# Performance work log

Hardware: AMD Instinct MI355X
Metric: run time of the kernel (lower is better)

Reference implementation:

```python
import jax, jax.numpy as jnp
import numpy as np
import math

N_HEAD = 16  # from init_kwargs

def setup_inputs() -> dict:
    key = jax.random.key(0)
    ks = jax.random.split(key, 11)
    B, T, D = 2, 2048, 1024
    s = 0.02
    return {
        "q": jax.random.normal(ks[0], (B, T, D), jnp.float32),
        "k": jax.random.normal(ks[1], (B, T, D), jnp.float32),
        "v": jax.random.normal(ks[2], (B, T, D), jnp.float32),
        "Wq": jax.random.normal(ks[3], (D, D), jnp.float32) * s,
        "bq": jax.random.normal(ks[4], (D,), jnp.float32) * s,
        "Wk": jax.random.normal(ks[5], (D, D), jnp.float32) * s,
        "bk": jax.random.normal(ks[6], (D,), jnp.float32) * s,
        "Wv": jax.random.normal(ks[7], (D, D), jnp.float32) * s,
        "bv": jax.random.normal(ks[8], (D,), jnp.float32) * s,
        "Wc": jax.random.normal(ks[9], (D, D), jnp.float32) * s,
        "bc": jax.random.normal(ks[10], (D,), jnp.float32) * s,
    }

def reference(q, k, v, Wq, bq, Wk, bk, Wv, bv, Wc, bc):
    B, T, D = q.shape
    H = N_HEAD
    nd = D // H

    def proj(x, W, b):
        # torch Linear: x @ W.T + b; then split heads -> [b, h, t, nd]
        y = x @ W.T + b
        return y.reshape(B, T, H, nd).transpose(0, 2, 1, 3)

    qh = proj(q, Wq, bq)
    kh = proj(k, Wk, bk)
    vh = proj(v, Wv, bv)

    # scores: [b, h, t_q, t_k]
    z = jnp.einsum('bhqd,bhkd->bhqk', qh, kh) / math.sqrt(nd)
    mask = jnp.tril(jnp.ones((T, T), dtype=bool))  # causal
    z = jnp.where(mask, z, -jnp.inf)
    # NOTE: original uses nn.Softmax(dim=-2) -> softmax over the QUERY axis
    attn = jax.nn.softmax(z, axis=-2)
    out = jnp.einsum('bhqk,bhkd->bhqd', attn, vh)  # [b, h, t, nd]
    out = out.transpose(0, 2, 1, 3).reshape(B, T, D)
    return out @ Wc.T + bc
```

## Files before the change

### kernel.cpp

```cpp
#include <hip/hip_runtime.h>


#define Dd 1024
#define Tt 2048
#define Bb 2
#define Hh 16
#define NDh 64
#define Mm (Bb * Tt)
#define LOG2E 1.44269504f

using u16 = unsigned short;
using u32 = unsigned int;
typedef __attribute__((ext_vector_type(8))) short bf16x8;
typedef __attribute__((ext_vector_type(4))) short bf16x4;
typedef __attribute__((ext_vector_type(4))) float f32x4;

__device__ __forceinline__ u16 f2bf(float f) {
  return (u16)((__float_as_uint(f) + 0x8000u) >> 16);
}
__device__ __forceinline__ float exp2_hw(float x) {
  float r; asm("v_exp_f32 %0, %1" : "=v"(r) : "v"(x)); return r;
}
__device__ __forceinline__ u32 cvtpk(float lo, float hi) {
  u32 r; asm("v_cvt_pk_bf16_f32 %0, %1, %2" : "=v"(r) : "v"(lo), "v"(hi));
  return r;
}
__device__ __forceinline__ void ldsdma16(const u16* g, u16* l) {
  __builtin_amdgcn_global_load_lds(
      (const __attribute__((address_space(1))) u32*)g,
      (__attribute__((address_space(3))) u32*)l, 16, 0, 0);
}
#define MFMA(a, b, c) __builtin_amdgcn_mfma_f32_16x16x32_bf16((a), (b), (c), 0, 0, 0)
__device__ __forceinline__ f32x4 mfma16(bf16x4 a, bf16x4 b, f32x4 c) {
#if __has_builtin(__builtin_amdgcn_mfma_f32_16x16x16bf16_1k)
  return __builtin_amdgcn_mfma_f32_16x16x16bf16_1k(a, b, c, 0, 0, 0);
#else
  f32x4 d;
  asm("v_mfma_f32_16x16x16_bf16 %0, %1, %2, %3"
      : "=v"(d) : "v"(a), "v"(b), "0"(c));
  return d;
#endif
}
__device__ __forceinline__ bf16x8 ldfrag(const u16* lds, int row, int kgrp) {
  return *(const bf16x8*)(lds + row * 64 + (((kgrp) ^ (row & 7)) * 8));
}
__device__ __forceinline__ bf16x4 ldv4(const u16* lds, int row, int e0) {
  return *(const bf16x4*)(lds + row * 64 + (((e0 >> 3) ^ (row & 7)) * 8) + (e0 & 7));
}

__global__ __launch_bounds__(256) void cvt_all(
    const float* __restrict__ w0, const float* __restrict__ w1,
    const float* __restrict__ w2, const float* __restrict__ w3,
    const float* __restrict__ xq, const float* __restrict__ xk,
    const float* __restrict__ xv,
    u16* __restrict__ Wb, u16* __restrict__ Qb, u16* __restrict__ Kb,
    u16* __restrict__ Vb, float* __restrict__ outz, float* __restrict__ lsumz)
{
  const int vid = blockIdx.x * 256 + threadIdx.x;
  const int seg = vid >> 18;
  const size_t off = (size_t)(vid & 0x3FFFF) * 4;
  const float* s;
  u16* d;
  if (seg < 4) {
    s = seg == 0 ? w0 : seg == 1 ? w1 : seg == 2 ? w2 : w3;
    d = Wb + (size_t)seg * Dd * Dd;
  } else {
    const int xi = (seg - 4) >> 2;
    const size_t xo = (size_t)((seg - 4) & 3) << 20;
    s = (xi == 0 ? xq : xi == 1 ? xk : xv) + xo;
    d = (xi == 0 ? Qb : xi == 1 ? Kb : Vb) + xo;
  }
  float4 f = *(const float4*)(s + off);
  ushort4 o;
  o.x = f2bf(f.x); o.y = f2bf(f.y); o.z = f2bf(f.z); o.w = f2bf(f.w);
  *(ushort4*)(d + off) = o;
  if (vid < Mm * Dd / 4)
    *(float4*)(outz + (size_t)vid * 4) = make_float4(0.f, 0.f, 0.f, 0.f);
  if (vid < Bb * Hh * Tt / 4)
    *(float4*)(lsumz + (size_t)vid * 4) = make_float4(0.f, 0.f, 0.f, 0.f);
}

__device__ __forceinline__ void gemm_body(
    const u16* __restrict__ X, const u16* __restrict__ WB,
    const float* __restrict__ bias, void* Yv, float oscale, int omode,
    int kc, int knum, u16* As, u16* Bs)
{
  const int t = threadIdx.x, lane = t & 63, w = t >> 6;
  const int col = lane & 15, quad = lane >> 4;
  const int m0 = blockIdx.x * 64, n0 = blockIdx.y * 128;
  const int wm = (w >> 1) * 32, wn = (w & 1) * 64;
  const int drr = lane >> 3, dsw = ((lane & 7) ^ drr) * 8;
  const int kbeg = (Dd / knum) * kc, kend = kbeg + Dd / knum;

  f32x4 acc[2][4] = {};

  for (int k0 = kbeg; k0 < kend; k0 += 64) {
    __syncthreads();
#pragma unroll
    for (int i = 0; i < 2; i++) {
      const int rr = w * 16 + i * 8;
      ldsdma16(X + (size_t)(m0 + rr + drr) * Dd + k0 + dsw, As + rr * 64);
    }
#pragma unroll
    for (int i = 0; i < 4; i++) {
      const int rr = w * 32 + i * 8;
      ldsdma16(WB + (size_t)(n0 + rr + drr) * Dd + k0 + dsw, Bs + rr * 64);
    }
    __syncthreads();
#pragma unroll
    for (int s = 0; s < 2; s++) {
      bf16x8 a[2], b[4];
#pragma unroll
      for (int i = 0; i < 2; i++)
        a[i] = ldfrag(As, wm + i * 16 + col, s * 4 + quad);
#pragma unroll
      for (int j = 0; j < 4; j++)
        b[j] = ldfrag(Bs, wn + j * 16 + col, s * 4 + quad);
#pragma unroll
      for (int i = 0; i < 2; i++)
#pragma unroll
        for (int j = 0; j < 4; j++)
          acc[i][j] = MFMA(a[i], b[j], acc[i][j]);
    }
  }

#pragma unroll
  for (int jt = 0; jt < 4; jt++) {
    const int n = n0 + wn + jt * 16 + col;
    const float bn = (omode == 2 && kc != 0) ? 0.f : bias[n];
    if (omode == 1) {
#pragma unroll
      for (int i = 0; i < 2; i++) {
        const int mg = m0 + wm + i * 16 + quad * 4;
        const int bb = mg >> 11, tl = mg & 2047;
        ushort4 o;
        o.x = f2bf(acc[i][jt][0] + bn);
        o.y = f2bf(acc[i][jt][1] + bn);
        o.z = f2bf(acc[i][jt][2] + bn);
        o.w = f2bf(acc[i][jt][3] + bn);
        *(ushort4*)((u16*)Yv + (size_t)bb * Dd * Tt + (size_t)n * Tt + tl) = o;
      }
    } else if (omode == 0) {
      u16* Y = (u16*)Yv;
#pragma unroll
      for (int i = 0; i < 2; i++)
#pragma unroll
        for (int r = 0; r < 4; r++) {
          const int m = m0 + wm + i * 16 + quad * 4 + r;
          Y[(size_t)m * Dd + n] = f2bf((acc[i][jt][r] + bn) * oscale);
        }
    } else {
      float* Y = (float*)Yv;
#pragma unroll
      for (int i = 0; i < 2; i++)
#pragma unroll
        for (int r = 0; r < 4; r++) {
          const int m = m0 + wm + i * 16 + quad * 4 + r;
          atomicAdd(&Y[(size_t)m * Dd + n], acc[i][jt][r] + bn);
        }
    }
  }
}

__global__ __launch_bounds__(256) void proj_qkv(
    const u16* __restrict__ Qb, const u16* __restrict__ Kb,
    const u16* __restrict__ Vb, const u16* __restrict__ Wb,
    const float* __restrict__ bq, const float* __restrict__ bk,
    const float* __restrict__ bv,
    u16* __restrict__ Qp, u16* __restrict__ Kp, u16* __restrict__ VtG)
{
  __shared__ u16 As[64 * 64];
  __shared__ u16 Bs[128 * 64];
  const int z = blockIdx.z;
  const u16* X = z == 0 ? Qb : z == 1 ? Kb : Vb;
  const u16* W = Wb + (size_t)z * Dd * Dd;
  const float* bias = z == 0 ? bq : z == 1 ? bk : bv;
  void* Y = z == 0 ? (void*)Qp : z == 1 ? (void*)Kp : (void*)VtG;
  gemm_body(X, W, bias, Y, z == 0 ? 0.125f * LOG2E : 1.0f, z == 2 ? 1 : 0,
            0, 1, As, Bs);
}

__global__ __launch_bounds__(256) void gemm_final(
    const u16* __restrict__ Ctx, const u16* __restrict__ Wcb,
    const float* __restrict__ bc, float* __restrict__ out)
{
  __shared__ u16 As[64 * 64];
  __shared__ u16 Bs[128 * 64];
  gemm_body(Ctx, Wcb, bc, out, 1.0f, 2, blockIdx.z, 2, As, Bs);
}

__global__ __launch_bounds__(256) void attn_stats(
    const u16* __restrict__ Qp, const u16* __restrict__ Kp,
    float* __restrict__ lsum)
{
  __shared__ u16 Ks[128 * 64];
  __shared__ u16 Qs[64 * 64];
  const int t = threadIdx.x, lane = t & 63, w = t >> 6;
  const int col = lane & 15, quad = lane >> 4;
  const int bh = blockIdx.x, b = bh >> 4, h = bh & 15;
  const int j = blockIdx.y, tk0 = j * 128, c = blockIdx.z;
  const u16* Kbase = Kp + (size_t)b * Tt * Dd + h * NDh;
  const u16* Qbase = Qp + (size_t)b * Tt * Dd + h * NDh;
  const int drr = lane >> 3, dsw = ((lane & 7) ^ drr) * 8;

#pragma unroll
  for (int i = 0; i < 4; i++) {
    const int rr = w * 32 + i * 8;
    ldsdma16(Kbase + (size_t)(tk0 + rr + drr) * Dd + dsw, Ks + rr * 64);
  }
  __syncthreads();
  bf16x8 ka[2][2];
#pragma unroll
  for (int s2 = 0; s2 < 2; s2++) {
    const int row = w * 32 + s2 * 16 + col;
    ka[s2][0] = ldfrag(Ks, row, quad);
    ka[s2][1] = ldfrag(Ks, row, 4 + quad);
  }

  float l[2][4] = {};

  for (int d = 2 * j + c, i0 = 0; d < Tt / 64; d += 4, i0++) {
    const bool masked = (c < 2) && (i0 == 0);
    const int tq0 = d * 64;
    __syncthreads();
#pragma unroll
    for (int i = 0; i < 2; i++) {
      const int rr = w * 16 + i * 8;
      ldsdma16(Qbase + (size_t)(tq0 + rr + drr) * Dd + dsw, Qs + rr * 64);
    }
    __syncthreads();
#pragma unroll
    for (int jt = 0; jt < 4; jt++) {
      bf16x8 qb0 = ldfrag(Qs, jt * 16 + col, quad);
      bf16x8 qb1 = ldfrag(Qs, jt * 16 + col, 4 + quad);
      const int tq = tq0 + jt * 16 + col;
#pragma unroll
      for (int s2 = 0; s2 < 2; s2++) {
        f32x4 z = {};
        z = MFMA(ka[s2][0], qb0, z);
        z = MFMA(ka[s2][1], qb1, z);
#pragma unroll
        for (int r = 0; r < 4; r++) {
          float e = exp2_hw(z[r]);
          if (masked) {
            const int tk = tk0 + w * 32 + s2 * 16 + quad * 4 + r;
            e = (tq >= tk) ? e : 0.f;
          }
          l[s2][r] += e;
        }
      }
    }
  }

#pragma unroll
  for (int s2 = 0; s2 < 2; s2++)
#pragma unroll
    for (int r = 0; r < 4; r++) {
      float s = l[s2][r];
#pragma unroll
      for (int m = 1; m < 16; m <<= 1) s += __shfl_xor(s, m);
      if (col == 0)
        atomicAdd(&lsum[(size_t)bh * Tt + tk0 + w * 32 + s2 * 16 + quad * 4 + r], s);
    }
}

__global__ __launch_bounds__(256) void attn_out(
    const u16* __restrict__ Qp, const u16* __restrict__ Kp,
    const u16* __restrict__ VtG, const float* __restrict__ lsum,
    u16* __restrict__ Ctx)
{
  __shared__ u16 Ks[2][64 * 64];
  __shared__ u16 Vts[2][64 * 64];
  __shared__ float srl[2][64];
  const int t = threadIdx.x, lane = t & 63, w = t >> 6;
  const int col = lane & 15, quad = lane >> 4;
  const int bh = blockIdx.x, b = bh >> 4, h = bh & 15;
  const int tq0 = (gridDim.y - 1 - blockIdx.y) * 64;
  const u16* Qbase = Qp + (size_t)b * Tt * Dd + h * NDh;
  const u16* Kbase = Kp + (size_t)b * Tt * Dd + h * NDh;
  const u16* Vbase = VtG + (size_t)b * Dd * Tt + (size_t)h * NDh * Tt;
  const int drr = lane >> 3, dsw = ((lane & 7) ^ drr) * 8;

#pragma unroll
  for (int i = 0; i < 2; i++) {
    const int rr = w * 16 + i * 8;
    ldsdma16(Qbase + (size_t)(tq0 + rr + drr) * Dd + dsw, Ks[0] + rr * 64);
  }
  __syncthreads();
  bf16x8 qa0 = ldfrag(Ks[0], w * 16 + col, quad);
  bf16x8 qa1 = ldfrag(Ks[0], w * 16 + col, 4 + quad);

  f32x4 o[4] = {};

  auto compute = [&](const u16* Kc, const u16* Vc, const float* rlc,
                     bool masked) {
#pragma unroll
    for (int jt = 0; jt < 4; jt++) {
      bf16x8 kb0 = ldfrag(Kc, jt * 16 + col, quad);
      bf16x8 kb1 = ldfrag(Kc, jt * 16 + col, 4 + quad);
      f32x4 z = {};
      z = MFMA(kb0, qa0, z);
      z = MFMA(kb1, qa1, z);
      const f32x4 rl = *(const f32x4*)(rlc + jt * 16 + quad * 4);
      float p0 = exp2_hw(z[0]) * rl[0];
      float p1 = exp2_hw(z[1]) * rl[1];
      float p2 = exp2_hw(z[2]) * rl[2];
      float p3 = exp2_hw(z[3]) * rl[3];
      if (masked) {
        const int tkb = jt * 16 + quad * 4, tq = w * 16 + col;
        p0 = (tkb + 0 <= tq) ? p0 : 0.f;
        p1 = (tkb + 1 <= tq) ? p1 : 0.f;
        p2 = (tkb + 2 <= tq) ? p2 : 0.f;
        p3 = (tkb + 3 <= tq) ? p3 : 0.f;
      }
      u32 pk01 = cvtpk(p0, p1), pk23 = cvtpk(p2, p3);
      u32 pkv[2] = {pk01, pk23};
      const bf16x4 pb2 = *(const bf16x4*)pkv;
#pragma unroll
      for (int dn = 0; dn < 4; dn++) {
        const bf16x4 va = ldv4(Vc, dn * 16 + col, jt * 16 + quad * 4);
        o[dn] = mfma16(va, pb2, o[dn]);
      }
    }
  };

  for (int tk0 = 0; tk0 <= tq0; tk0 += 128) {
    const bool two = (tk0 + 64 <= tq0);
    __syncthreads();
#pragma unroll
    for (int i = 0; i < 2; i++) {
      const int rr = w * 16 + i * 8;
      ldsdma16(Kbase + (size_t)(tk0 + rr + drr) * Dd + dsw, Ks[0] + rr * 64);
      ldsdma16(Vbase + (size_t)(rr + drr) * Tt + tk0 + dsw, Vts[0] + rr * 64);
    }
    if (two) {
#pragma unroll
      for (int i = 0; i < 2; i++) {
        const int rr = w * 16 + i * 8;
        ldsdma16(Kbase + (size_t)(tk0 + 64 + rr + drr) * Dd + dsw,
                 Ks[1] + rr * 64);
        ldsdma16(Vbase + (size_t)(rr + drr) * Tt + tk0 + 64 + dsw,
                 Vts[1] + rr * 64);
      }
    }
    if (t < 64) {
      srl[0][t] = 1.0f / lsum[(size_t)bh * Tt + tk0 + t];
      if (two) srl[1][t] = 1.0f / lsum[(size_t)bh * Tt + tk0 + 64 + t];
    }
    __syncthreads();
    compute(Ks[0], Vts[0], srl[0], tk0 == tq0);
    if (two) compute(Ks[1], Vts[1], srl[1], tk0 + 64 == tq0);
  }

#pragma unroll
  for (int dn = 0; dn < 4; dn++) {
    ushort4 ov;
    ov.x = f2bf(o[dn][0]); ov.y = f2bf(o[dn][1]);
    ov.z = f2bf(o[dn][2]); ov.w = f2bf(o[dn][3]);
    *(ushort4*)(Ctx + (size_t)(b * Tt + tq0 + w * 16 + col) * Dd +
                h * NDh + dn * 16 + quad * 4) = ov;
  }
}

extern "C" void kernel_launch(void* const* d_in, const int* in_sizes, int n_in,
                              void* d_out, int out_size, void* d_ws, size_t ws_size,
                              hipStream_t stream)
{
  const float* q  = (const float*)d_in[0];
  const float* k  = (const float*)d_in[1];
  const float* v  = (const float*)d_in[2];
  const float* Wq = (const float*)d_in[3];
  const float* bq = (const float*)d_in[4];
  const float* Wk = (const float*)d_in[5];
  const float* bk = (const float*)d_in[6];
  const float* Wv = (const float*)d_in[7];
  const float* bv = (const float*)d_in[8];
  const float* Wc = (const float*)d_in[9];
  const float* bc = (const float*)d_in[10];

  u16* Wb   = (u16*)d_ws;
  u16* Qp   = Wb + (size_t)4 * Dd * Dd;
  u16* Kp   = Qp + (size_t)Mm * Dd;
  u16* VtG  = Kp + (size_t)Mm * Dd;
  u16* Ctx  = VtG + (size_t)Mm * Dd;
  float* lsum = (float*)(Ctx + (size_t)Mm * Dd);
  u16* Qb   = (u16*)(lsum + (size_t)Bb * Hh * Tt);
  u16* Kb   = Qb + (size_t)Mm * Dd;
  u16* Vb   = Ctx;

  cvt_all<<<16384, 256, 0, stream>>>(Wq, Wk, Wv, Wc, q, k, v,
                                     Wb, Qb, Kb, Vb, (float*)d_out, lsum);
  proj_qkv<<<dim3(Mm / 64, Dd / 128, 3), 256, 0, stream>>>(
      Qb, Kb, Vb, Wb, bq, bk, bv, Qp, Kp, VtG);
  attn_stats<<<dim3(Bb * Hh, Tt / 128, 4), 256, 0, stream>>>(Qp, Kp, lsum);
  attn_out<<<dim3(Bb * Hh, Tt / 64), 256, 0, stream>>>(Qp, Kp, VtG, lsum, Ctx);
  gemm_final<<<dim3(Mm / 64, Dd / 128, 2), 256, 0, stream>>>(
      Ctx, Wb + (size_t)3 * Dd * Dd, bc, (float*)d_out);
}
```

Before: 257.9 us.

## Pair short and long causal query tiles per block in attn_out

Each attn_out block now handles two 64-row query tiles, p and 31-p, so every block does about the same causal work. The K/V tiles loaded into shared memory are reused for both query tiles, and the grid shrinks from 32 to 16 blocks per head. This removes tail imbalance and halves K/V reloads, but it doubles accumulator registers and leaves 512 blocks, which may hurt occupancy and latency hiding.

Result: no change. 257.8 us (-0.0%).

```diff
diff --git a/kernel.cpp b/kernel.cpp
--- a/kernel.cpp
+++ b/kernel.cpp
@@ -275,7 +275,8 @@
   const int t = threadIdx.x, lane = t & 63, w = t >> 6;
   const int col = lane & 15, quad = lane >> 4;
   const int bh = blockIdx.x, b = bh >> 4, h = bh & 15;
-  const int tq0 = (gridDim.y - 1 - blockIdx.y) * 64;
+  const int p = blockIdx.y;
+  const int tqA = p * 64, tqB = (31 - p) * 64;
   const u16* Qbase = Qp + (size_t)b * Tt * Dd + h * NDh;
   const u16* Kbase = Kp + (size_t)b * Tt * Dd + h * NDh;
   const u16* Vbase = VtG + (size_t)b * Dd * Tt + (size_t)h * NDh * Tt;
@@ -284,48 +285,76 @@
 #pragma unroll
   for (int i = 0; i < 2; i++) {
     const int rr = w * 16 + i * 8;
-    ldsdma16(Qbase + (size_t)(tq0 + rr + drr) * Dd + dsw, Ks[0] + rr * 64);
+    ldsdma16(Qbase + (size_t)(tqA + rr + drr) * Dd + dsw, Ks[0] + rr * 64);
+    ldsdma16(Qbase + (size_t)(tqB + rr + drr) * Dd + dsw, Ks[1] + rr * 64);
   }
   __syncthreads();
-  bf16x8 qa0 = ldfrag(Ks[0], w * 16 + col, quad);
-  bf16x8 qa1 = ldfrag(Ks[0], w * 16 + col, 4 + quad);
-
-  f32x4 o[4] = {};
-
-  auto compute = [&](const u16* Kc, const u16* Vc, const float* rlc,
-                     bool masked) {
+  bf16x8 qaA0 = ldfrag(Ks[0], w * 16 + col, quad);
+  bf16x8 qaA1 = ldfrag(Ks[0], w * 16 + col, 4 + quad);
+  bf16x8 qaB0 = ldfrag(Ks[1], w * 16 + col, quad);
+  bf16x8 qaB1 = ldfrag(Ks[1], w * 16 + col, 4 + quad);
+
+  f32x4 oA[4] = {}, oB[4] = {};
+
+  auto computePair = [&](const u16* Kc, const u16* Vc, const float* rlc,
+                         bool actA, bool mA, bool mB) {
 #pragma unroll
     for (int jt = 0; jt < 4; jt++) {
       bf16x8 kb0 = ldfrag(Kc, jt * 16 + col, quad);
       bf16x8 kb1 = ldfrag(Kc, jt * 16 + col, 4 + quad);
-      f32x4 z = {};
-      z = MFMA(kb0, qa0, z);
-      z = MFMA(kb1, qa1, z);
       const f32x4 rl = *(const f32x4*)(rlc + jt * 16 + quad * 4);
-      float p0 = exp2_hw(z[0]) * rl[0];
-      float p1 = exp2_hw(z[1]) * rl[1];
-      float p2 = exp2_hw(z[2]) * rl[2];
-      float p3 = exp2_hw(z[3]) * rl[3];
-      if (masked) {
-        const int tkb = jt * 16 + quad * 4, tq = w * 16 + col;
-        p0 = (tkb + 0 <= tq) ? p0 : 0.f;
-        p1 = (tkb + 1 <= tq) ? p1 : 0.f;
-        p2 = (tkb + 2 <= tq) ? p2 : 0.f;
-        p3 = (tkb + 3 <= tq) ? p3 : 0.f;
+      const int tkb = jt * 16 + quad * 4, tql = w * 16 + col;
+
+      f32x4 zB = {};
+      zB = MFMA(kb0, qaB0, zB);
+      zB = MFMA(kb1, qaB1, zB);
+      float pB0 = exp2_hw(zB[0]) * rl[0];
+      float pB1 = exp2_hw(zB[1]) * rl[1];
+      float pB2 = exp2_hw(zB[2]) * rl[2];
+      float pB3 = exp2_hw(zB[3]) * rl[3];
+      if (mB) {
+        pB0 = (tkb + 0 <= tql) ? pB0 : 0.f;
+        pB1 = (tkb + 1 <= tql) ? pB1 : 0.f;
+        pB2 = (tkb + 2 <= tql) ? pB2 : 0.f;
+        pB3 = (tkb + 3 <= tql) ? pB3 : 0.f;
       }
-      u32 pk01 = cvtpk(p0, p1), pk23 = cvtpk(p2, p3);
-      u32 pkv[2] = {pk01, pk23};
-      const bf16x4 pb2 = *(const bf16x4*)pkv;
-#pragma unroll
-      for (int dn = 0; dn < 4; dn++) {
-        const bf16x4 va = ldv4(Vc, dn * 16 + col, jt * 16 + quad * 4);
-        o[dn] = mfma16(va, pb2, o[dn]);
+      u32 pkB[2] = {cvtpk(pB0, pB1), cvtpk(pB2, pB3)};
+      const bf16x4 pbB = *(const bf16x4*)pkB;
+
+      if (actA) {
+        f32x4 zA = {};
+        zA = MFMA(kb0, qaA0, zA);
+        zA = MFMA(kb1, qaA1, zA);
+        float pA0 = exp2_hw(zA[0]) * rl[0];
+        float pA1 = exp2_hw(zA[1]) * rl[1];
+        float pA2 = exp2_hw(zA[2]) * rl[2];
+        float pA3 = exp2_hw(zA[3]) * rl[3];
+        if (mA) {
+          pA0 = (tkb + 0 <= tql) ? pA0 : 0.f;
+          pA1 = (tkb + 1 <= tql) ? pA1 : 0.f;
+          pA2 = (tkb + 2 <= tql) ? pA2 : 0.f;
+          pA3 = (tkb + 3 <= tql) ? pA3 : 0.f;
+        }
+        u32 pkA[2] = {cvtpk(pA0, pA1), cvtpk(pA2, pA3)};
+        const bf16x4 pbA = *(const bf16x4*)pkA;
+#pragma unroll
+        for (int dn = 0; dn < 4; dn++) {
+          const bf16x4 va = ldv4(Vc, dn * 16 + col, jt * 16 + quad * 4);
+          oB[dn] = mfma16(va, pbB, oB[dn]);
+          oA[dn] = mfma16(va, pbA, oA[dn]);
+        }
+      } else {
+#pragma unroll
+        for (int dn = 0; dn < 4; dn++) {
+          const bf16x4 va = ldv4(Vc, dn * 16 + col, jt * 16 + quad * 4);
+          oB[dn] = mfma16(va, pbB, oB[dn]);
+        }
       }
     }
   };
 
-  for (int tk0 = 0; tk0 <= tq0; tk0 += 128) {
-    const bool two = (tk0 + 64 <= tq0);
+  for (int tk0 = 0; tk0 <= tqB; tk0 += 128) {
+    const bool two = (tk0 + 64 <= tqB);
     __syncthreads();
 #pragma unroll
     for (int i = 0; i < 2; i++) {
@@ -348,17 +377,22 @@
       if (two) srl[1][t] = 1.0f / lsum[(size_t)bh * Tt + tk0 + 64 + t];
     }
     __syncthreads();
-    compute(Ks[0], Vts[0], srl[0], tk0 == tq0);
-    if (two) compute(Ks[1], Vts[1], srl[1], tk0 + 64 == tq0);
+    computePair(Ks[0], Vts[0], srl[0], tk0 <= tqA, tk0 == tqA, tk0 == tqB);
+    if (two)
+      computePair(Ks[1], Vts[1], srl[1], tk0 + 64 <= tqA, tk0 + 64 == tqA,
+                  tk0 + 64 == tqB);
   }
 
 #pragma unroll
   for (int dn = 0; dn < 4; dn++) {
-    ushort4 ov;
-    ov.x = f2bf(o[dn][0]); ov.y = f2bf(o[dn][1]);
-    ov.z = f2bf(o[dn][2]); ov.w = f2bf(o[dn][3]);
-    *(ushort4*)(Ctx + (size_t)(b * Tt + tq0 + w * 16 + col) * Dd +
-                h * NDh + dn * 16 + quad * 4) = ov;
+    ushort4 ovA, ovB;
+    ovA.x = f2bf(oA[dn][0]); ovA.y = f2bf(oA[dn][1]);
+    ovA.z = f2bf(oA[dn][2]); ovA.w = f2bf(oA[dn][3]);
+    ovB.x = f2bf(oB[dn][0]); ovB.y = f2bf(oB[dn][1]);
+    ovB.z = f2bf(oB[dn][2]); ovB.w = f2bf(oB[dn][3]);
+    const int nn = h * NDh + dn * 16 + quad * 4;
+    *(ushort4*)(Ctx + (size_t)(b * Tt + tqA + w * 16 + col) * Dd + nn) = ovA;
+    *(ushort4*)(Ctx + (size_t)(b * Tt + tqB + w * 16 + col) * Dd + nn) = ovB;
   }
 }
 
@@ -393,7 +427,7 @@
   proj_qkv<<<dim3(Mm / 64, Dd / 128, 3), 256, 0, stream>>>(
       Qb, Kb, Vb, Wb, bq, bk, bv, Qp, Kp, VtG);
   attn_stats<<<dim3(Bb * Hh, Tt / 128, 4), 256, 0, stream>>>(Qp, Kp, lsum);
-  attn_out<<<dim3(Bb * Hh, Tt / 64), 256, 0, stream>>>(Qp, Kp, VtG, lsum, Ctx);
+  attn_out<<<dim3(Bb * Hh, 16), 256, 0, stream>>>(Qp, Kp, VtG, lsum, Ctx);
   gemm_final<<<dim3(Mm / 64, Dd / 128, 2), 256, 0, stream>>>(
       Ctx, Wb + (size_t)3 * Dd * Dd, bc, (float*)d_out);
 }
```
